# Optimization experiments

Hardware: AMD Instinct MI355X
Metric: run time of the kernel (lower is better)

The kernel has to match this reference:

```python
import jax, jax.numpy as jnp
import numpy as np

B = 1_000_000          # query points
D = 3                  # n_input_dims
N_LEVELS = 16
MIN_RES, MAX_RES = 16, 512
N_ENC = 2 ** 19        # max hashmap entries per level
N_EMBED = 2
INIT_SCALE = 1e-4
PRIMES = (1, 2654435761, 805459861)  # instant-ngp spatial-hash primes


def _resolutions():
    # Eq. 2/3 of instant-ngp: geometric growth from MIN_RES to MAX_RES
    growth = np.exp((np.log(MAX_RES) - np.log(MIN_RES)) / (N_LEVELS - 1))
    return [int(np.floor(MIN_RES * growth ** l)) for l in range(N_LEVELS)]

RES = _resolutions()
LEVEL_N_ENC = [min(r ** D, N_ENC) for r in RES]
LEVEL_HASH = [r ** D > N_ENC for r in RES]          # hash iff grid overflows table
CORNERS = np.stack(np.meshgrid(*([np.arange(2)] * D), indexing='ij'), -1).reshape(-1, D)  # (8,3)


def setup_inputs() -> dict:
    key = jax.random.key(0)
    ks = jax.random.split(key, N_LEVELS + 1)
    inp = {"x": jax.random.uniform(ks[0], (B, D), minval=-1.0, maxval=1.0, dtype=jnp.float32)}
    for l in range(N_LEVELS):
        inp[f"emb{l}"] = jax.random.uniform(
            ks[l + 1], (LEVEL_N_ENC[l], N_EMBED), minval=-INIT_SCALE, maxval=INIT_SCALE, dtype=jnp.float32
        )
    return inp


def _level_features(x, emb, res, n_enc, use_hash):
    # x: (B,3) in [-1,1] -> pixel coords, align_corners=False convention
    xp = (x + 1.0) * (res * 0.5) - 0.5
    x0 = jnp.floor(xp)
    t = xp - x0                                           # (B,3) fractional part
    ci = jnp.asarray(CORNERS, jnp.int32)                  # (8,3) corner offsets
    c = x0.astype(jnp.int32)[:, None, :] + ci[None]       # (B,8,3) corner coords
    off = jnp.asarray(CORNERS, xp.dtype)
    # trilinear weights: prod over dims of t or (1-t)
    w = jnp.prod(jnp.where(off[None] > 0, t[:, None, :], 1.0 - t[:, None, :]), axis=-1)  # (B,8)
    m = jnp.all((c >= 0) & (c < res), axis=-1)            # (B,8) zeros-padding mask
    if use_hash:
        cu = c.astype(jnp.uint32)
        h = cu[..., 0] * jnp.uint32(PRIMES[0])
        for d in range(1, D):
            h = h ^ (cu[..., d] * jnp.uint32(PRIMES[d]))
        ids = (h % jnp.uint32(n_enc)).astype(jnp.int32)
    else:
        # ravel index, x varies fastest ('xy' grid indexing)
        ids = (c[..., 0] + c[..., 1] * res + c[..., 2] * res * res) % n_enc
    ids = jnp.where(m, ids, 0)
    w = jnp.where(m, w, jnp.zeros_like(w))
    return jnp.sum(emb[ids] * w[..., None], axis=1)       # (B,E)


def reference(x, emb0, emb1, emb2, emb3, emb4, emb5, emb6, emb7,
              emb8, emb9, emb10, emb11, emb12, emb13, emb14, emb15):
    embs = [emb0, emb1, emb2, emb3, emb4, emb5, emb6, emb7,
            emb8, emb9, emb10, emb11, emb12, emb13, emb14, emb15]
    feats = [_level_features(x, embs[l], RES[l], LEVEL_N_ENC[l], LEVEL_HASH[l])
             for l in range(N_LEVELS)]
    return jnp.stack(feats, axis=1)  # (B, L, E)
```

## Files before the change

kernel.cpp:

```cpp
#include <hip/hip_runtime.h>
#include <stdint.h>


struct EmbPtrs { const float2* p[16]; };

constexpr int BLOCK = 256;
constexpr int kRes[16] = {16,20,25,32,40,50,64,80,101,128,161,203,256,322,406,512};
constexpr uint32_t P1 = 2654435761u, P2 = 805459861u;
constexpr uint32_t HMASK = (1u << 19) - 1u;

struct Tri {
    int ix, iy, iz;
    float wx[2], wy[2], wz[2];
    bool vx[2], vy[2], vz[2];
};

template<int RES_>
__device__ __forceinline__ Tri tri_setup(float px, float py, float pz)
{
    Tri s;
    const float rh = (float)RES_ * 0.5f;
    const float xp = (px + 1.0f) * rh - 0.5f;
    const float yp = (py + 1.0f) * rh - 0.5f;
    const float zp = (pz + 1.0f) * rh - 0.5f;
    const float fx = floorf(xp), fy = floorf(yp), fz = floorf(zp);
    s.ix = (int)fx; s.iy = (int)fy; s.iz = (int)fz;
    const float tx = xp - fx, ty = yp - fy, tz = zp - fz;
    s.wx[0] = 1.0f - tx; s.wx[1] = tx;
    s.wy[0] = 1.0f - ty; s.wy[1] = ty;
    s.wz[0] = 1.0f - tz; s.wz[1] = tz;
    s.vx[0] = (s.ix   >= 0) && (s.ix   < RES_); s.vx[1] = (s.ix+1 >= 0) && (s.ix+1 < RES_);
    s.vy[0] = (s.iy   >= 0) && (s.iy   < RES_); s.vy[1] = (s.iy+1 >= 0) && (s.iy+1 < RES_);
    s.vz[0] = (s.iz   >= 0) && (s.iz   < RES_); s.vz[1] = (s.iz+1 >= 0) && (s.iz+1 < RES_);
    return s;
}

template<int RES_>
__device__ __forceinline__ float2 dense_feat(const float2* __restrict__ tab,
                                             float px, float py, float pz)
{
    const Tri s = tri_setup<RES_>(px, py, pz);
    constexpr int r2 = RES_ * RES_;
    const int base = s.ix + s.iy * RES_ + s.iz * r2;
    float ax = 0.0f, ay = 0.0f;
#pragma unroll
    for (int k = 0; k < 2; ++k)
#pragma unroll
    for (int j = 0; j < 2; ++j) {
        const bool vyz = s.vy[j] && s.vz[k];
        const float wyz = s.wy[j] * s.wz[k];
        const int i0 = base + j * RES_ + k * r2;
        const float w0 = (vyz && s.vx[0]) ? s.wx[0] * wyz : 0.0f;
        const float w1 = (vyz && s.vx[1]) ? s.wx[1] * wyz : 0.0f;
        if (vyz && s.vx[0] && s.vx[1] && !(i0 & 1)) {
            const float4 q = *(const float4*)(tab + i0);
            ax = fmaf(q.x, w0, ax); ay = fmaf(q.y, w0, ay);
            ax = fmaf(q.z, w1, ax); ay = fmaf(q.w, w1, ay);
        } else {
            const uint32_t a0 = (vyz && s.vx[0]) ? (uint32_t)i0       : 0u;
            const uint32_t a1 = (vyz && s.vx[1]) ? (uint32_t)(i0 + 1) : 0u;
            const float2 e0 = tab[a0];
            const float2 e1 = tab[a1];
            ax = fmaf(e0.x, w0, ax); ay = fmaf(e0.y, w0, ay);
            ax = fmaf(e1.x, w1, ax); ay = fmaf(e1.y, w1, ay);
        }
    }
    return make_float2(ax, ay);
}

template<int RES_>
__device__ __forceinline__ float2 hash_feat(const float2* __restrict__ tab,
                                            float px, float py, float pz)
{
    const Tri s = tri_setup<RES_>(px, py, pz);
    const uint32_t hy0 = (uint32_t)s.iy * P1;
    const uint32_t hz0 = (uint32_t)s.iz * P2;
    const uint32_t hy[2] = {hy0, hy0 + P1};
    const uint32_t hz[2] = {hz0, hz0 + P2};
    const uint32_t ux = (uint32_t)s.ix;
    float ax = 0.0f, ay = 0.0f;
#pragma unroll
    for (int k = 0; k < 2; ++k)
#pragma unroll
    for (int j = 0; j < 2; ++j) {
        const bool vyz = s.vy[j] && s.vz[k];
        const float wyz = s.wy[j] * s.wz[k];
        const uint32_t E = hy[j] ^ hz[k];
        const uint32_t J0 = (ux ^ E) & HMASK;
        const uint32_t J1 = ((ux + 1u) ^ E) & HMASK;
        const float w0 = (vyz && s.vx[0]) ? s.wx[0] * wyz : 0.0f;
        const float w1 = (vyz && s.vx[1]) ? s.wx[1] * wyz : 0.0f;
        if (!(ux & 1u)) {
            const float4 q = *(const float4*)(tab + (J0 & ~1u));
            const float wl = (J0 & 1u) ? w1 : w0;
            const float wh = (J0 & 1u) ? w0 : w1;
            ax = fmaf(q.x, wl, ax); ay = fmaf(q.y, wl, ay);
            ax = fmaf(q.z, wh, ax); ay = fmaf(q.w, wh, ay);
        } else {
            const float2 e0 = tab[J0];
            const float2 e1 = tab[J1];
            ax = fmaf(e0.x, w0, ax); ay = fmaf(e0.y, w0, ay);
            ax = fmaf(e1.x, w1, ax); ay = fmaf(e1.y, w1, ay);
        }
    }
    return make_float2(ax, ay);
}

__global__ __launch_bounds__(BLOCK) void dense_kernel(
    const float* __restrict__ x, EmbPtrs embs, float4* __restrict__ out, int n)
{
    const int b = blockIdx.x * BLOCK + threadIdx.x;
    if (b >= n) return;
    const float px = x[3*b+0], py = x[3*b+1], pz = x[3*b+2];

    float2 f[8];
    f[0] = dense_feat<16>(embs.p[0], px, py, pz);
    f[1] = dense_feat<20>(embs.p[1], px, py, pz);
    f[2] = dense_feat<25>(embs.p[2], px, py, pz);
    f[3] = dense_feat<32>(embs.p[3], px, py, pz);
    f[4] = dense_feat<40>(embs.p[4], px, py, pz);
    f[5] = dense_feat<50>(embs.p[5], px, py, pz);
    f[6] = dense_feat<64>(embs.p[6], px, py, pz);
    f[7] = dense_feat<80>(embs.p[7], px, py, pz);

    float4* o = out + (size_t)b * 8;
#pragma unroll
    for (int i = 0; i < 4; ++i)
        o[i] = make_float4(f[2*i].x, f[2*i].y, f[2*i+1].x, f[2*i+1].y);
}

template<int L>
__global__ __launch_bounds__(BLOCK) void hash_level_kernel(
    const float* __restrict__ x, const float2* __restrict__ tab,
    float2* __restrict__ ws, int n)
{
    const int h = (n + 1) >> 1;
    const int b = blockIdx.x * BLOCK + threadIdx.x;
    if (b >= h) return;
    ws[b] = hash_feat<kRes[L]>(tab, x[3*b+0], x[3*b+1], x[3*b+2]);
    const int p1 = b + h;
    if (p1 < n)
        ws[p1] = hash_feat<kRes[L]>(tab, x[3*p1+0], x[3*p1+1], x[3*p1+2]);
}

__global__ __launch_bounds__(BLOCK) void merge_kernel2(
    const float2* __restrict__ ws, float4* __restrict__ out, int n)
{
    const int t = blockIdx.x * BLOCK + threadIdx.x;
    if (t >= (n >> 1)) return;
    const int p0 = 2 * t;
    float4 q[8];
#pragma unroll
    for (int l = 0; l < 8; ++l)
        q[l] = *(const float4*)(ws + (size_t)l * n + p0);
    float4* o0 = out + (size_t)p0 * 8 + 4;
    float4* o1 = out + (size_t)(p0 + 1) * 8 + 4;
#pragma unroll
    for (int i = 0; i < 4; ++i) {
        o0[i] = make_float4(q[2*i].x, q[2*i].y, q[2*i+1].x, q[2*i+1].y);
        o1[i] = make_float4(q[2*i].z, q[2*i].w, q[2*i+1].z, q[2*i+1].w);
    }
}

__global__ __launch_bounds__(BLOCK) void merge_kernel1(
    const float2* __restrict__ ws, float4* __restrict__ out, int n)
{
    const int b = blockIdx.x * BLOCK + threadIdx.x;
    if (b >= n) return;
    float2 f[8];
#pragma unroll
    for (int l = 0; l < 8; ++l)
        f[l] = ws[(size_t)l * n + b];
    float4* o = out + (size_t)b * 8 + 4;
#pragma unroll
    for (int i = 0; i < 4; ++i)
        o[i] = make_float4(f[2*i].x, f[2*i].y, f[2*i+1].x, f[2*i+1].y);
}

__global__ __launch_bounds__(BLOCK) void fallback_kernel(
    const float* __restrict__ x, EmbPtrs embs, float4* __restrict__ out, int n)
{
    const int b = blockIdx.x * BLOCK + threadIdx.x;
    if (b >= n) return;
    const float px = x[3*b+0], py = x[3*b+1], pz = x[3*b+2];
    float2 f[16];
    f[0]  = dense_feat<16 >(embs.p[0],  px, py, pz);
    f[1]  = dense_feat<20 >(embs.p[1],  px, py, pz);
    f[2]  = dense_feat<25 >(embs.p[2],  px, py, pz);
    f[3]  = dense_feat<32 >(embs.p[3],  px, py, pz);
    f[4]  = dense_feat<40 >(embs.p[4],  px, py, pz);
    f[5]  = dense_feat<50 >(embs.p[5],  px, py, pz);
    f[6]  = dense_feat<64 >(embs.p[6],  px, py, pz);
    f[7]  = dense_feat<80 >(embs.p[7],  px, py, pz);
    f[8]  = hash_feat<101>(embs.p[8],  px, py, pz);
    f[9]  = hash_feat<128>(embs.p[9],  px, py, pz);
    f[10] = hash_feat<161>(embs.p[10], px, py, pz);
    f[11] = hash_feat<203>(embs.p[11], px, py, pz);
    f[12] = hash_feat<256>(embs.p[12], px, py, pz);
    f[13] = hash_feat<322>(embs.p[13], px, py, pz);
    f[14] = hash_feat<406>(embs.p[14], px, py, pz);
    f[15] = hash_feat<512>(embs.p[15], px, py, pz);
    float4* o = out + (size_t)b * 8;
#pragma unroll
    for (int i = 0; i < 8; ++i)
        o[i] = make_float4(f[2*i].x, f[2*i].y, f[2*i+1].x, f[2*i+1].y);
}

extern "C" void kernel_launch(void* const* d_in, const int* in_sizes, int n_in,
                              void* d_out, int out_size, void* d_ws, size_t ws_size,
                              hipStream_t stream) {
    const float* x = (const float*)d_in[0];
    EmbPtrs embs;
    for (int l = 0; l < 16; ++l) embs.p[l] = (const float2*)d_in[1 + l];
    const int n = in_sizes[0] / 3;
    const int grid  = (n + BLOCK - 1) / BLOCK;
    const int hgrid = (((n + 1) >> 1) + BLOCK - 1) / BLOCK;
    float4* out = (float4*)d_out;

    const size_t need = (size_t)8 * (size_t)n * sizeof(float2);
    if (ws_size >= need) {
        float2* ws = (float2*)d_ws;
        dense_kernel<<<grid, BLOCK, 0, stream>>>(x, embs, out, n);
        hash_level_kernel< 8><<<hgrid, BLOCK, 0, stream>>>(x, embs.p[ 8], ws + 0*(size_t)n, n);
        hash_level_kernel< 9><<<hgrid, BLOCK, 0, stream>>>(x, embs.p[ 9], ws + 1*(size_t)n, n);
        hash_level_kernel<10><<<hgrid, BLOCK, 0, stream>>>(x, embs.p[10], ws + 2*(size_t)n, n);
        hash_level_kernel<11><<<hgrid, BLOCK, 0, stream>>>(x, embs.p[11], ws + 3*(size_t)n, n);
        hash_level_kernel<12><<<hgrid, BLOCK, 0, stream>>>(x, embs.p[12], ws + 4*(size_t)n, n);
        hash_level_kernel<13><<<hgrid, BLOCK, 0, stream>>>(x, embs.p[13], ws + 5*(size_t)n, n);
        hash_level_kernel<14><<<hgrid, BLOCK, 0, stream>>>(x, embs.p[14], ws + 6*(size_t)n, n);
        hash_level_kernel<15><<<hgrid, BLOCK, 0, stream>>>(x, embs.p[15], ws + 7*(size_t)n, n);
        if ((n & 1) == 0)
            merge_kernel2<<<hgrid, BLOCK, 0, stream>>>(ws, out, n);
        else
            merge_kernel1<<<grid, BLOCK, 0, stream>>>(ws, out, n);
    } else {
        fallback_kernel<<<grid, BLOCK, 0, stream>>>(x, embs, out, n);
    }
}
```

Measured before the change: 708.5 us.

## Stage small dense tables in LDS, simplify gathers, drop two-point hash threads

The dense kernel now runs with 1024-thread blocks and first copies the level-0 and level-1 embedding tables into shared memory, then reads those two levels from LDS. Dense and hash gathers drop the paired float4 fast path in favour of one float2 load per corner. The hash-level kernels go from two points per thread to one, and the even-n vectorised merge is replaced by the simple per-point merge. The intent is to cut global gather traffic and code complexity. In exchange it loses the wider loads and adds a per-block table-copy prologue plus lower occupancy from larger blocks and LDS use.

```diff
diff --git a/kernel.cpp b/kernel.cpp
--- a/kernel.cpp
+++ b/kernel.cpp
@@ -4,7 +4,10 @@
 
 struct EmbPtrs { const float2* p[16]; };
 
-constexpr int BLOCK = 256;
+constexpr int BLOCK  = 256;
+constexpr int DBLOCK = 1024;
+constexpr int L0N = 16*16*16;
+constexpr int L1N = 20*20*20;
 constexpr int kRes[16] = {16,20,25,32,40,50,64,80,101,128,161,203,256,322,406,512};
 constexpr uint32_t P1 = 2654435761u, P2 = 805459861u;
 constexpr uint32_t HMASK = (1u << 19) - 1u;
@@ -35,9 +38,8 @@
     return s;
 }
 
-template<int RES_>
-__device__ __forceinline__ float2 dense_feat(const float2* __restrict__ tab,
-                                             float px, float py, float pz)
+template<int RES_, typename PTR>
+__device__ __forceinline__ float2 dense_feat(PTR tab, float px, float py, float pz)
 {
     const Tri s = tri_setup<RES_>(px, py, pz);
     constexpr int r2 = RES_ * RES_;
@@ -46,24 +48,15 @@
 #pragma unroll
     for (int k = 0; k < 2; ++k)
 #pragma unroll
-    for (int j = 0; j < 2; ++j) {
-        const bool vyz = s.vy[j] && s.vz[k];
-        const float wyz = s.wy[j] * s.wz[k];
-        const int i0 = base + j * RES_ + k * r2;
-        const float w0 = (vyz && s.vx[0]) ? s.wx[0] * wyz : 0.0f;
-        const float w1 = (vyz && s.vx[1]) ? s.wx[1] * wyz : 0.0f;
-        if (vyz && s.vx[0] && s.vx[1] && !(i0 & 1)) {
-            const float4 q = *(const float4*)(tab + i0);
-            ax = fmaf(q.x, w0, ax); ay = fmaf(q.y, w0, ay);
-            ax = fmaf(q.z, w1, ax); ay = fmaf(q.w, w1, ay);
-        } else {
-            const uint32_t a0 = (vyz && s.vx[0]) ? (uint32_t)i0       : 0u;
-            const uint32_t a1 = (vyz && s.vx[1]) ? (uint32_t)(i0 + 1) : 0u;
-            const float2 e0 = tab[a0];
-            const float2 e1 = tab[a1];
-            ax = fmaf(e0.x, w0, ax); ay = fmaf(e0.y, w0, ay);
-            ax = fmaf(e1.x, w1, ax); ay = fmaf(e1.y, w1, ay);
-        }
+    for (int j = 0; j < 2; ++j)
+#pragma unroll
+    for (int i = 0; i < 2; ++i) {
+        const bool v = s.vx[i] && s.vy[j] && s.vz[k];
+        const uint32_t idx = v ? (uint32_t)(base + i + j*RES_ + k*r2) : 0u;
+        const float w = v ? (s.wx[i]*s.wy[j]*s.wz[k]) : 0.0f;
+        const float2 e = tab[idx];
+        ax = fmaf(e.x, w, ax);
+        ay = fmaf(e.y, w, ay);
     }
     return make_float2(ax, ay);
 }
@@ -75,47 +68,52 @@
     const Tri s = tri_setup<RES_>(px, py, pz);
     const uint32_t hy0 = (uint32_t)s.iy * P1;
     const uint32_t hz0 = (uint32_t)s.iz * P2;
+    const uint32_t hx[2] = {(uint32_t)s.ix, (uint32_t)s.ix + 1u};
     const uint32_t hy[2] = {hy0, hy0 + P1};
     const uint32_t hz[2] = {hz0, hz0 + P2};
-    const uint32_t ux = (uint32_t)s.ix;
     float ax = 0.0f, ay = 0.0f;
 #pragma unroll
     for (int k = 0; k < 2; ++k)
 #pragma unroll
-    for (int j = 0; j < 2; ++j) {
-        const bool vyz = s.vy[j] && s.vz[k];
-        const float wyz = s.wy[j] * s.wz[k];
-        const uint32_t E = hy[j] ^ hz[k];
-        const uint32_t J0 = (ux ^ E) & HMASK;
-        const uint32_t J1 = ((ux + 1u) ^ E) & HMASK;
-        const float w0 = (vyz && s.vx[0]) ? s.wx[0] * wyz : 0.0f;
-        const float w1 = (vyz && s.vx[1]) ? s.wx[1] * wyz : 0.0f;
-        if (!(ux & 1u)) {
-            const float4 q = *(const float4*)(tab + (J0 & ~1u));
-            const float wl = (J0 & 1u) ? w1 : w0;
-            const float wh = (J0 & 1u) ? w0 : w1;
-            ax = fmaf(q.x, wl, ax); ay = fmaf(q.y, wl, ay);
-            ax = fmaf(q.z, wh, ax); ay = fmaf(q.w, wh, ay);
-        } else {
-            const float2 e0 = tab[J0];
-            const float2 e1 = tab[J1];
-            ax = fmaf(e0.x, w0, ax); ay = fmaf(e0.y, w0, ay);
-            ax = fmaf(e1.x, w1, ax); ay = fmaf(e1.y, w1, ay);
-        }
+    for (int j = 0; j < 2; ++j)
+#pragma unroll
+    for (int i = 0; i < 2; ++i) {
+        const bool v = s.vx[i] && s.vy[j] && s.vz[k];
+        uint32_t idx = (hx[i] ^ hy[j] ^ hz[k]) & HMASK;
+        idx = v ? idx : 0u;
+        const float w = v ? (s.wx[i]*s.wy[j]*s.wz[k]) : 0.0f;
+        const float2 e = tab[idx];
+        ax = fmaf(e.x, w, ax);
+        ay = fmaf(e.y, w, ay);
     }
     return make_float2(ax, ay);
 }
 
-__global__ __launch_bounds__(BLOCK) void dense_kernel(
+__global__ __launch_bounds__(DBLOCK) void dense_kernel(
     const float* __restrict__ x, EmbPtrs embs, float4* __restrict__ out, int n)
 {
-    const int b = blockIdx.x * BLOCK + threadIdx.x;
+    __shared__ float2 lds0[L0N];
+    __shared__ float2 lds1[L1N];
+
+    {
+        const float4* g0 = (const float4*)embs.p[0];
+        const float4* g1 = (const float4*)embs.p[1];
+        float4* s0 = (float4*)lds0;
+        float4* s1 = (float4*)lds1;
+#pragma unroll 2
+        for (int i = threadIdx.x; i < L0N/2; i += DBLOCK) s0[i] = g0[i];
+#pragma unroll 4
+        for (int i = threadIdx.x; i < L1N/2; i += DBLOCK) s1[i] = g1[i];
+    }
+    __syncthreads();
+
+    const int b = blockIdx.x * DBLOCK + threadIdx.x;
     if (b >= n) return;
     const float px = x[3*b+0], py = x[3*b+1], pz = x[3*b+2];
 
     float2 f[8];
-    f[0] = dense_feat<16>(embs.p[0], px, py, pz);
-    f[1] = dense_feat<20>(embs.p[1], px, py, pz);
+    f[0] = dense_feat<16>((const float2*)lds0, px, py, pz);
+    f[1] = dense_feat<20>((const float2*)lds1, px, py, pz);
     f[2] = dense_feat<25>(embs.p[2], px, py, pz);
     f[3] = dense_feat<32>(embs.p[3], px, py, pz);
     f[4] = dense_feat<40>(embs.p[4], px, py, pz);
@@ -134,35 +132,12 @@
     const float* __restrict__ x, const float2* __restrict__ tab,
     float2* __restrict__ ws, int n)
 {
-    const int h = (n + 1) >> 1;
     const int b = blockIdx.x * BLOCK + threadIdx.x;
-    if (b >= h) return;
+    if (b >= n) return;
     ws[b] = hash_feat<kRes[L]>(tab, x[3*b+0], x[3*b+1], x[3*b+2]);
-    const int p1 = b + h;
-    if (p1 < n)
-        ws[p1] = hash_feat<kRes[L]>(tab, x[3*p1+0], x[3*p1+1], x[3*p1+2]);
-}
-
-__global__ __launch_bounds__(BLOCK) void merge_kernel2(
-    const float2* __restrict__ ws, float4* __restrict__ out, int n)
-{
-    const int t = blockIdx.x * BLOCK + threadIdx.x;
-    if (t >= (n >> 1)) return;
-    const int p0 = 2 * t;
-    float4 q[8];
-#pragma unroll
-    for (int l = 0; l < 8; ++l)
-        q[l] = *(const float4*)(ws + (size_t)l * n + p0);
-    float4* o0 = out + (size_t)p0 * 8 + 4;
-    float4* o1 = out + (size_t)(p0 + 1) * 8 + 4;
-#pragma unroll
-    for (int i = 0; i < 4; ++i) {
-        o0[i] = make_float4(q[2*i].x, q[2*i].y, q[2*i+1].x, q[2*i+1].y);
-        o1[i] = make_float4(q[2*i].z, q[2*i].w, q[2*i+1].z, q[2*i+1].w);
-    }
-}
-
-__global__ __launch_bounds__(BLOCK) void merge_kernel1(
+}
+
+__global__ __launch_bounds__(BLOCK) void merge_kernel(
     const float2* __restrict__ ws, float4* __restrict__ out, int n)
 {
     const int b = blockIdx.x * BLOCK + threadIdx.x;
@@ -214,25 +189,22 @@
     for (int l = 0; l < 16; ++l) embs.p[l] = (const float2*)d_in[1 + l];
     const int n = in_sizes[0] / 3;
     const int grid  = (n + BLOCK - 1) / BLOCK;
-    const int hgrid = (((n + 1) >> 1) + BLOCK - 1) / BLOCK;
+    const int dgrid = (n + DBLOCK - 1) / DBLOCK;
     float4* out = (float4*)d_out;
 
     const size_t need = (size_t)8 * (size_t)n * sizeof(float2);
     if (ws_size >= need) {
         float2* ws = (float2*)d_ws;
-        dense_kernel<<<grid, BLOCK, 0, stream>>>(x, embs, out, n);
-        hash_level_kernel< 8><<<hgrid, BLOCK, 0, stream>>>(x, embs.p[ 8], ws + 0*(size_t)n, n);
-        hash_level_kernel< 9><<<hgrid, BLOCK, 0, stream>>>(x, embs.p[ 9], ws + 1*(size_t)n, n);
-        hash_level_kernel<10><<<hgrid, BLOCK, 0, stream>>>(x, embs.p[10], ws + 2*(size_t)n, n);
-        hash_level_kernel<11><<<hgrid, BLOCK, 0, stream>>>(x, embs.p[11], ws + 3*(size_t)n, n);
-        hash_level_kernel<12><<<hgrid, BLOCK, 0, stream>>>(x, embs.p[12], ws + 4*(size_t)n, n);
-        hash_level_kernel<13><<<hgrid, BLOCK, 0, stream>>>(x, embs.p[13], ws + 5*(size_t)n, n);
-        hash_level_kernel<14><<<hgrid, BLOCK, 0, stream>>>(x, embs.p[14], ws + 6*(size_t)n, n);
-        hash_level_kernel<15><<<hgrid, BLOCK, 0, stream>>>(x, embs.p[15], ws + 7*(size_t)n, n);
-        if ((n & 1) == 0)
-            merge_kernel2<<<hgrid, BLOCK, 0, stream>>>(ws, out, n);
-        else
-            merge_kernel1<<<grid, BLOCK, 0, stream>>>(ws, out, n);
+        dense_kernel<<<dgrid, DBLOCK, 0, stream>>>(x, embs, out, n);
+        hash_level_kernel< 8><<<grid, BLOCK, 0, stream>>>(x, embs.p[ 8], ws + 0*(size_t)n, n);
+        hash_level_kernel< 9><<<grid, BLOCK, 0, stream>>>(x, embs.p[ 9], ws + 1*(size_t)n, n);
+        hash_level_kernel<10><<<grid, BLOCK, 0, stream>>>(x, embs.p[10], ws + 2*(size_t)n, n);
+        hash_level_kernel<11><<<grid, BLOCK, 0, stream>>>(x, embs.p[11], ws + 3*(size_t)n, n);
+        hash_level_kernel<12><<<grid, BLOCK, 0, stream>>>(x, embs.p[12], ws + 4*(size_t)n, n);
+        hash_level_kernel<13><<<grid, BLOCK, 0, stream>>>(x, embs.p[13], ws + 5*(size_t)n, n);
+        hash_level_kernel<14><<<grid, BLOCK, 0, stream>>>(x, embs.p[14], ws + 6*(size_t)n, n);
+        hash_level_kernel<15><<<grid, BLOCK, 0, stream>>>(x, embs.p[15], ws + 7*(size_t)n, n);
+        merge_kernel<<<grid, BLOCK, 0, stream>>>(ws, out, n);
     } else {
         fallback_kernel<<<grid, BLOCK, 0, stream>>>(x, embs, out, n);
     }
```

Result: faster. 636.0 us (-10.2%).
